# Kernel tuning notes

Measured on AMD Instinct MI355X. Metric: run time of the kernel, lower is better.

## Reference

```python
import jax, jax.numpy as jnp
import numpy as np

B, N, F, K = 16384, 64, 128, 64


def setup_inputs() -> dict:
    key = jax.random.key(0)
    kx, kd = jax.random.split(key)
    x = jax.random.normal(kx, (B, F), dtype=jnp.float32)
    D = jax.random.normal(kd, (N, F, K), dtype=jnp.float32)  # per-cluster factor dictionaries
    return {"x": x, "D": D}


def reference(x, D):
    # --- assignment step (torch.no_grad in original) ---
    # Dtx[n,b,j] = sum_i D[n,i,j] * x[b,i]
    Dtx = jnp.einsum('nij,bi->nbj', D, x)                      # [N,B,K]
    # per-cluster (D^T D)^{-1}, batched inverse over the cluster axis
    DTD = jnp.einsum('nij,nik->njk', D, D)                     # [N,K,K]
    DTD_inv = jnp.linalg.inv(DTD)                              # [N,K,K]
    Cs = jnp.einsum('nbj,nkj->nbk', Dtx, DTD_inv)              # [N,B,K]
    x_hat = jnp.einsum('nij,nbj->nbi', D, Cs)                  # [N,B,F]
    # nearest-subspace assignment per sample
    label = jnp.argmin(jnp.linalg.norm(x_hat - x[None], axis=-1), axis=0)  # [B] int
    C = Cs[label, jnp.arange(x.shape[0])]                      # [B,K] gather per sample
    # --- reconstruction loss: sum_i || x[i] - D[label[i]] @ C[i] ||^2 ---
    x_rec = jnp.einsum('bik,bk->bi', D[label], C)              # grouped gather + matmul
    se_loss = jnp.sum(jnp.square(x - x_rec))
    return se_loss, label
```

## Files before the change

### kernel.cpp

```cpp
#include <hip/hip_runtime.h>
#include <hip/hip_bf16.h>

#define B_N 16384
#define TAU 0.25f
#define GS 68
#define YS 132

typedef float f32x4 __attribute__((ext_vector_type(4)));
typedef short s16x8 __attribute__((ext_vector_type(8)));

__device__ __forceinline__ void gl_lds16(const void* g, void* l) {
    __builtin_amdgcn_global_load_lds(
        (const __attribute__((address_space(1))) void*)g,
        (__attribute__((address_space(3))) void*)l, 16, 0, 0);
}

__device__ __forceinline__ unsigned short bf16_bits(float v) {
    __hip_bfloat16 h = __float2bfloat16(v);
    return *reinterpret_cast<unsigned short*>(&h);
}

__global__ __launch_bounds__(256) void prep_convert(const float* __restrict__ x,
                                                    const float* __restrict__ D,
                                                    unsigned short* __restrict__ xh,
                                                    float* __restrict__ nrm,
                                                    float* __restrict__ Qg,
                                                    unsigned short* __restrict__ Bht,
                                                    float* __restrict__ out) {
    __shared__ __align__(16) float Y[64 * YS];
    __shared__ __align__(16) float G[64 * GS + 64];
    __shared__ __align__(16) float Lti[8 * 8 * 8];
    const int t = threadIdx.x;

    if (blockIdx.x >= 64) {
        const int gid = (blockIdx.x - 64) * 256 + t;
        if (gid == 0) out[0] = 0.0f;
        const size_t base = (size_t)gid * 64;
        float s = 0.0f;
        #pragma unroll
        for (int c = 0; c < 16; ++c) {
            const f32x4 v = ((const f32x4*)(x + base))[c];
            s += v.x * v.x + v.y * v.y + v.z * v.z + v.w * v.w;
            ushort4 h;
            h.x = bf16_bits(v.x); h.y = bf16_bits(v.y);
            h.z = bf16_bits(v.z); h.w = bf16_bits(v.w);
            ((ushort4*)(xh + base))[c] = h;
        }
        s += __shfl_xor(s, 1, 64);
        if ((gid & 1) == 0) nrm[gid >> 1] = s;
        return;
    }

    const int n = blockIdx.x;
    const float* Dn = D + (size_t)n * 8192;

    for (int e4 = t; e4 < 2048; e4 += 256) {
        const int c = e4 >> 4, j4 = (e4 & 15) * 4;
        const f32x4 v = ((const f32x4*)Dn)[e4];
        Y[(j4 + 0) * YS + c] = v.x;
        Y[(j4 + 1) * YS + c] = v.y;
        Y[(j4 + 2) * YS + c] = v.z;
        Y[(j4 + 3) * YS + c] = v.w;
    }
    __syncthreads();

    {
        const int a0 = (t & 15) * 4, b0 = (t >> 4) * 4;
        float acc[4][4] = {};
        for (int c4 = 0; c4 < 32; ++c4) {
            f32x4 A[4], Bv[4];
            #pragma unroll
            for (int p = 0; p < 4; ++p) {
                A[p]  = *(const f32x4*)&Y[(a0 + p) * YS + c4 * 4];
                Bv[p] = *(const f32x4*)&Y[(b0 + p) * YS + c4 * 4];
            }
            #pragma unroll
            for (int p = 0; p < 4; ++p)
                #pragma unroll
                for (int q = 0; q < 4; ++q)
                    acc[p][q] += A[p].x * Bv[q].x + A[p].y * Bv[q].y +
                                 A[p].z * Bv[q].z + A[p].w * Bv[q].w;
        }
        #pragma unroll
        for (int p = 0; p < 4; ++p)
            #pragma unroll
            for (int q = 0; q < 4; ++q) G[(a0 + p) * GS + b0 + q] = acc[p][q];
    }
    __syncthreads();

    for (int p8 = 0; p8 < 8; ++p8) {
        const int pb = p8 * 8;
        if (t < 64) {
            const int lane = t;
            const f32x4 v0 = *(const f32x4*)&G[lane * GS + pb];
            const f32x4 v1 = *(const f32x4*)&G[lane * GS + pb + 4];
            float g[8] = {v0.x, v0.y, v0.z, v0.w, v1.x, v1.y, v1.z, v1.w};
            #pragma unroll
            for (int kk = 0; kk < 8; ++kk) {
                const int k = pb + kk;
                const float dk = __shfl(g[kk], k, 64);
                const float rinv = 1.0f / sqrtf(dk);
                const float lik = g[kk] * rinv;
                g[kk] = lik;
                if (lane == 0) G[64 * GS + k] = rinv;
                #pragma unroll
                for (int jj = kk + 1; jj < 8; ++jj) {
                    const float ljk = __shfl(lik, pb + jj, 64);
                    g[jj] -= lik * ljk;
                }
            }
            *(f32x4*)&G[lane * GS + pb]     = (f32x4){g[0], g[1], g[2], g[3]};
            *(f32x4*)&G[lane * GS + pb + 4] = (f32x4){g[4], g[5], g[6], g[7]};
        }
        __syncthreads();
        const int base = pb + 8;
        if (base < 64) {
            for (int i = base + (t >> 5); i < 64; i += 8) {
                const f32x4 Li0 = *(const f32x4*)&G[i * GS + pb];
                const f32x4 Li1 = *(const f32x4*)&G[i * GS + pb + 4];
                for (int j = base + (t & 31); j < 64; j += 32) {
                    const f32x4 Lj0 = *(const f32x4*)&G[j * GS + pb];
                    const f32x4 Lj1 = *(const f32x4*)&G[j * GS + pb + 4];
                    float s = G[i * GS + j];
                    s -= Li0.x * Lj0.x + Li0.y * Lj0.y + Li0.z * Lj0.z + Li0.w * Lj0.w;
                    s -= Li1.x * Lj1.x + Li1.y * Lj1.y + Li1.z * Lj1.z + Li1.w * Lj1.w;
                    G[i * GS + j] = s;
                }
            }
        }
        __syncthreads();
    }

    if (t < 64) {
        const int bi = t >> 3, c = t & 7;
        const int base = bi * 8;
        float m[8];
        #pragma unroll
        for (int r = 0; r < 8; ++r) {
            float s = (r == c) ? 1.0f : 0.0f;
            #pragma unroll
            for (int k = 0; k < r; ++k)
                s -= G[(base + r) * GS + base + k] * m[k];
            m[r] = s * G[64 * GS + base + r];
        }
        #pragma unroll
        for (int r = 0; r < 8; ++r) Lti[(base + r) * 8 + c] = m[r];
    }
    __syncthreads();

    if (t < 128) {
        const int c = t;
        for (int i = 0; i < 8; ++i) {
            float Tv[8];
            #pragma unroll
            for (int r = 0; r < 8; ++r) Tv[r] = Y[(i * 8 + r) * YS + c];
            for (int k = 0; k < i; ++k) {
                #pragma unroll
                for (int kk = 0; kk < 8; ++kk) {
                    const float z = Y[(k * 8 + kk) * YS + c];
                    #pragma unroll
                    for (int r = 0; r < 8; ++r)
                        Tv[r] -= G[(i * 8 + r) * GS + k * 8 + kk] * z;
                }
            }
            #pragma unroll
            for (int r = 0; r < 8; ++r) {
                float z = 0.0f;
                #pragma unroll
                for (int rp = 0; rp <= r; ++rp)
                    z += Lti[(i * 8 + r) * 8 + rp] * Tv[rp];
                Y[(i * 8 + r) * YS + c] = z;
            }
        }
    }
    __syncthreads();

    for (int e = t; e < 8192; e += 256) {
        const int j = e >> 7, i = e & 127;
        Bht[((size_t)n * 64 + j) * 128 + i] = bf16_bits(Y[j * YS + i]);
    }
    for (int e = t; e < 8192; e += 256) {
        const int i = e >> 6, j = e & 63;
        Qg[(size_t)n * 8192 + e] = Y[j * YS + i];
    }
}

__global__ __launch_bounds__(256) void gemm_scores(const unsigned short* __restrict__ xh,
                                                   const unsigned short* __restrict__ Bht,
                                                   float* __restrict__ S) {
    __shared__ unsigned short ldsA[128 * 128];
    __shared__ unsigned short ldsB[128 * 128];
    const int t = threadIdx.x, w = t >> 6, lane = t & 63;
    const int m0 = blockIdx.x * 128;
    const int nsplit = blockIdx.y;
    const int wm = w & 1, wn = w >> 1;

    {
        const int rl = lane >> 4;
        const int p  = lane & 15;
        #pragma unroll
        for (int q = 0; q < 8; ++q) {
            const int row = w * 32 + q * 4 + rl;
            const int c = p ^ (row & 15);
            gl_lds16(xh + (size_t)(m0 + row) * 128 + c * 8,
                     &ldsA[(w * 32 + q * 4) * 128]);
            gl_lds16(Bht + (size_t)(nsplit * 1024 + row) * 128 + c * 8,
                     &ldsB[(w * 32 + q * 4) * 128]);
        }
    }
    __syncthreads();

    s16x8 af[4][4];
    #pragma unroll
    for (int mt = 0; mt < 4; ++mt) {
        const int r = wm * 64 + mt * 16 + (lane & 15);
        #pragma unroll
        for (int ks = 0; ks < 4; ++ks) {
            const int p = (ks * 4 + (lane >> 4)) ^ (lane & 15);
            af[mt][ks] = *(const s16x8*)&ldsA[r * 128 + p * 8];
        }
    }

    #pragma unroll 1
    for (int it = 0; it < 8; ++it) {
        s16x8 bf[4][4];
        #pragma unroll
        for (int nt = 0; nt < 4; ++nt) {
            const int r = wn * 64 + nt * 16 + (lane & 15);
            #pragma unroll
            for (int ks = 0; ks < 4; ++ks) {
                const int p = (ks * 4 + (lane >> 4)) ^ (lane & 15);
                bf[nt][ks] = *(const s16x8*)&ldsB[r * 128 + p * 8];
            }
        }
        __syncthreads();

        if (it < 7) {
            const int rl = lane >> 4, p = lane & 15;
            #pragma unroll
            for (int q = 0; q < 8; ++q) {
                const int row = w * 32 + q * 4 + rl;
                const int c = p ^ (row & 15);
                gl_lds16(Bht + (size_t)(nsplit * 1024 + (it + 1) * 128 + row) * 128 + c * 8,
                         &ldsB[(w * 32 + q * 4) * 128]);
            }
        }

        f32x4 acc[4][4];
        #pragma unroll
        for (int mt = 0; mt < 4; ++mt)
            #pragma unroll
            for (int nt = 0; nt < 4; ++nt) acc[mt][nt] = (f32x4){0.f, 0.f, 0.f, 0.f};
        #pragma unroll
        for (int ks = 0; ks < 4; ++ks)
            #pragma unroll
            for (int mt = 0; mt < 4; ++mt)
                #pragma unroll
                for (int nt = 0; nt < 4; ++nt)
                    acc[mt][nt] = __builtin_amdgcn_mfma_f32_16x16x32_bf16(
                        af[mt][ks], bf[nt][ks], acc[mt][nt], 0, 0, 0);

        const int nc = nsplit * 16 + it * 2 + wn;
        #pragma unroll
        for (int mt = 0; mt < 4; ++mt) {
            #pragma unroll
            for (int rg = 0; rg < 4; ++rg) {
                float p = 0.0f;
                #pragma unroll
                for (int nt = 0; nt < 4; ++nt) {
                    const float v = acc[mt][nt][rg];
                    p += v * v;
                }
                p += __shfl_xor(p, 1, 64);
                p += __shfl_xor(p, 2, 64);
                p += __shfl_xor(p, 4, 64);
                p += __shfl_xor(p, 8, 64);
                if ((lane & 15) == 0) {
                    const int m = wm * 64 + mt * 16 + (lane >> 4) * 4 + rg;
                    S[(size_t)nc * B_N + m0 + m] = p;
                }
            }
        }
        __syncthreads();
    }
}

__global__ __launch_bounds__(256) void argmax_rescore(const float* __restrict__ Sa,
                                                      const float* __restrict__ nrm,
                                                      const float* __restrict__ x,
                                                      const float* __restrict__ Qg,
                                                      float* __restrict__ out) {
    __shared__ float tile[64 * 65];
    __shared__ int sflags[64];
    __shared__ int scnt;
    __shared__ float ssum;
    __shared__ float scorr[4];
    const int t = threadIdx.x, w = t >> 6, lane = t & 63;
    const int b0 = blockIdx.x * 64;
    if (t == 0) scnt = 0;

    for (int idx = t; idx < 1024; idx += 256) {
        const int n = idx >> 4, c4 = idx & 15;
        const f32x4 v = *(const f32x4*)&Sa[(size_t)n * B_N + b0 + c4 * 4];
        tile[(c4 * 4 + 0) * 65 + n] = v.x;
        tile[(c4 * 4 + 1) * 65 + n] = v.y;
        tile[(c4 * 4 + 2) * 65 + n] = v.z;
        tile[(c4 * 4 + 3) * 65 + n] = v.w;
    }
    __syncthreads();

    if (t < 64) {
        float v1 = -1e30f, v2 = -1e30f;
        int n1 = 0;
        for (int n = 0; n < 64; ++n) {
            const float v = tile[t * 65 + n];
            if (v > v1) { v2 = v1; v1 = v; n1 = n; }
            else v2 = fmaxf(v2, v);
        }
        out[1 + b0 + t] = (float)n1;
        if (v1 - v2 < TAU) { const int i = atomicAdd(&scnt, 1); sflags[i] = t; }
        float err = nrm[b0 + t] - v1;
        for (int off = 32; off; off >>= 1) err += __shfl_xor(err, off, 64);
        if (t == 0) ssum = err;
    }
    if (lane == 0) scorr[w] = 0.0f;
    __syncthreads();

    const int nf = scnt;
    float corr = 0.0f;
    for (int f = w; f < nf; f += 4) {
        const int s = sflags[f];
        const int b2 = b0 + s;
        const float v = tile[s * 65 + lane];
        float vm = v;
        for (int off = 32; off; off >>= 1) vm = fmaxf(vm, __shfl_xor(vm, off, 64));
        unsigned long long mask = __ballot((vm - v) < TAU);
        float best = -1e30f;
        int bn = 0;
        while (mask) {
            const int nn = (int)__builtin_ctzll(mask);
            mask &= mask - 1;
            const float* Qn = Qg + (size_t)nn * 8192;
            const float* xb = x + (size_t)b2 * 128;
            float dot = 0.0f;
            #pragma unroll 8
            for (int i = 0; i < 128; ++i)
                dot = fmaf(Qn[i * 64 + lane], xb[i], dot);
            float sv = dot * dot;
            for (int off = 32; off; off >>= 1) sv += __shfl_xor(sv, off, 64);
            if (sv > best) { best = sv; bn = nn; }
        }
        if (lane == 0) {
            out[1 + b2] = (float)bn;
            corr += vm - best;
        }
    }
    if (lane == 0 && corr != 0.0f) scorr[w] += corr;
    __syncthreads();
    if (t == 0)
        atomicAdd(out, ssum + scorr[0] + scorr[1] + scorr[2] + scorr[3]);
}

extern "C" void kernel_launch(void* const* d_in, const int* in_sizes, int n_in,
                              void* d_out, int out_size, void* d_ws, size_t ws_size,
                              hipStream_t stream) {
    const float* x = (const float*)d_in[0];
    const float* D = (const float*)d_in[1];
    float* out = (float*)d_out;

    char* ws = (char*)d_ws;
    unsigned short* xh  = (unsigned short*)(ws);
    unsigned short* Bht = (unsigned short*)(ws + (4u << 20));
    float* Qg           = (float*)(ws + (5u << 20));
    float* Sa           = (float*)(ws + (7u << 20));
    float* nrm          = (float*)(ws + (11u << 20));

    prep_convert<<<192, 256, 0, stream>>>(x, D, xh, nrm, Qg, Bht, out);
    gemm_scores<<<dim3(128, 4), 256, 0, stream>>>(xh, Bht, Sa);
    argmax_rescore<<<256, 256, 0, stream>>>(Sa, nrm, x, Qg, out);
}
```

Before: 164.1 us.

## Split prep kernel, compute Gram from global, shrink MFMA accumulator live range

The combined prep/convert kernel is split into two launches: a convert kernel in which each thread handles 32 floats, and a per-cluster prep kernel. The D^T D Gram product now reads D directly from global memory with scalar FMAs, so the LDS transpose no longer feeds it and the barrier after the transpose is dropped. The Y pad changes to 133. In gemm_scores, MFMA accumulation moves inside the per-mt loop so only 4 accumulators stay live, which is meant to lower register pressure. The trade-offs are an extra kernel launch, and later readers of Y may lose the synchronisation they relied on.

```diff
diff --git a/kernel.cpp b/kernel.cpp
--- a/kernel.cpp
+++ b/kernel.cpp
@@ -4,7 +4,7 @@
 #define B_N 16384
 #define TAU 0.25f
 #define GS 68
-#define YS 132
+#define YS 133
 
 typedef float f32x4 __attribute__((ext_vector_type(4)));
 typedef short s16x8 __attribute__((ext_vector_type(8)));
@@ -20,37 +20,35 @@
     return *reinterpret_cast<unsigned short*>(&h);
 }
 
-__global__ __launch_bounds__(256) void prep_convert(const float* __restrict__ x,
-                                                    const float* __restrict__ D,
-                                                    unsigned short* __restrict__ xh,
-                                                    float* __restrict__ nrm,
-                                                    float* __restrict__ Qg,
-                                                    unsigned short* __restrict__ Bht,
-                                                    float* __restrict__ out) {
-    __shared__ __align__(16) float Y[64 * YS];
+__global__ __launch_bounds__(256) void convert_kernel(const float* __restrict__ x,
+                                                      unsigned short* __restrict__ xh,
+                                                      float* __restrict__ nrm,
+                                                      float* __restrict__ out) {
+    const int gid = blockIdx.x * 256 + threadIdx.x;
+    if (gid == 0) out[0] = 0.0f;
+    const size_t base = (size_t)gid * 32;
+    float s = 0.0f;
+    #pragma unroll
+    for (int c = 0; c < 8; ++c) {
+        const f32x4 v = ((const f32x4*)(x + base))[c];
+        s += v.x * v.x + v.y * v.y + v.z * v.z + v.w * v.w;
+        ushort4 h;
+        h.x = bf16_bits(v.x); h.y = bf16_bits(v.y);
+        h.z = bf16_bits(v.z); h.w = bf16_bits(v.w);
+        ((ushort4*)(xh + base))[c] = h;
+    }
+    s += __shfl_xor(s, 1, 64);
+    s += __shfl_xor(s, 2, 64);
+    if ((gid & 3) == 0) nrm[gid >> 2] = s;
+}
+
+__global__ __launch_bounds__(256) void prep_kernel(const float* __restrict__ D,
+                                                   float* __restrict__ Qg,
+                                                   unsigned short* __restrict__ Bht) {
+    __shared__ float Y[64 * YS];
     __shared__ __align__(16) float G[64 * GS + 64];
     __shared__ __align__(16) float Lti[8 * 8 * 8];
     const int t = threadIdx.x;
-
-    if (blockIdx.x >= 64) {
-        const int gid = (blockIdx.x - 64) * 256 + t;
-        if (gid == 0) out[0] = 0.0f;
-        const size_t base = (size_t)gid * 64;
-        float s = 0.0f;
-        #pragma unroll
-        for (int c = 0; c < 16; ++c) {
-            const f32x4 v = ((const f32x4*)(x + base))[c];
-            s += v.x * v.x + v.y * v.y + v.z * v.z + v.w * v.w;
-            ushort4 h;
-            h.x = bf16_bits(v.x); h.y = bf16_bits(v.y);
-            h.z = bf16_bits(v.z); h.w = bf16_bits(v.w);
-            ((ushort4*)(xh + base))[c] = h;
-        }
-        s += __shfl_xor(s, 1, 64);
-        if ((gid & 1) == 0) nrm[gid >> 1] = s;
-        return;
-    }
-
     const int n = blockIdx.x;
     const float* Dn = D + (size_t)n * 8192;
 
@@ -62,24 +60,20 @@
         Y[(j4 + 2) * YS + c] = v.z;
         Y[(j4 + 3) * YS + c] = v.w;
     }
-    __syncthreads();
 
     {
         const int a0 = (t & 15) * 4, b0 = (t >> 4) * 4;
         float acc[4][4] = {};
-        for (int c4 = 0; c4 < 32; ++c4) {
-            f32x4 A[4], Bv[4];
-            #pragma unroll
-            for (int p = 0; p < 4; ++p) {
-                A[p]  = *(const f32x4*)&Y[(a0 + p) * YS + c4 * 4];
-                Bv[p] = *(const f32x4*)&Y[(b0 + p) * YS + c4 * 4];
-            }
+        #pragma unroll 4
+        for (int i = 0; i < 128; ++i) {
+            const f32x4 av = *(const f32x4*)(Dn + i * 64 + a0);
+            const f32x4 bv = *(const f32x4*)(Dn + i * 64 + b0);
+            const float aa[4] = {av.x, av.y, av.z, av.w};
+            const float bb[4] = {bv.x, bv.y, bv.z, bv.w};
             #pragma unroll
             for (int p = 0; p < 4; ++p)
                 #pragma unroll
-                for (int q = 0; q < 4; ++q)
-                    acc[p][q] += A[p].x * Bv[q].x + A[p].y * Bv[q].y +
-                                 A[p].z * Bv[q].z + A[p].w * Bv[q].w;
+                for (int q = 0; q < 4; ++q) acc[p][q] = fmaf(aa[p], bb[q], acc[p][q]);
         }
         #pragma unroll
         for (int p = 0; p < 4; ++p)
@@ -246,29 +240,24 @@
             }
         }
 
-        f32x4 acc[4][4];
-        #pragma unroll
-        for (int mt = 0; mt < 4; ++mt)
-            #pragma unroll
-            for (int nt = 0; nt < 4; ++nt) acc[mt][nt] = (f32x4){0.f, 0.f, 0.f, 0.f};
-        #pragma unroll
-        for (int ks = 0; ks < 4; ++ks)
-            #pragma unroll
-            for (int mt = 0; mt < 4; ++mt)
+        const int nc = nsplit * 16 + it * 2 + wn;
+        #pragma unroll
+        for (int mt = 0; mt < 4; ++mt) {
+            f32x4 acc[4];
+            #pragma unroll
+            for (int nt = 0; nt < 4; ++nt) acc[nt] = (f32x4){0.f, 0.f, 0.f, 0.f};
+            #pragma unroll
+            for (int ks = 0; ks < 4; ++ks)
                 #pragma unroll
                 for (int nt = 0; nt < 4; ++nt)
-                    acc[mt][nt] = __builtin_amdgcn_mfma_f32_16x16x32_bf16(
-                        af[mt][ks], bf[nt][ks], acc[mt][nt], 0, 0, 0);
-
-        const int nc = nsplit * 16 + it * 2 + wn;
-        #pragma unroll
-        for (int mt = 0; mt < 4; ++mt) {
+                    acc[nt] = __builtin_amdgcn_mfma_f32_16x16x32_bf16(
+                        af[mt][ks], bf[nt][ks], acc[nt], 0, 0, 0);
             #pragma unroll
             for (int rg = 0; rg < 4; ++rg) {
                 float p = 0.0f;
                 #pragma unroll
                 for (int nt = 0; nt < 4; ++nt) {
-                    const float v = acc[mt][nt][rg];
+                    const float v = acc[nt][rg];
                     p += v * v;
                 }
                 p += __shfl_xor(p, 1, 64);
@@ -375,7 +364,8 @@
     float* Sa           = (float*)(ws + (7u << 20));
     float* nrm          = (float*)(ws + (11u << 20));
 
-    prep_convert<<<192, 256, 0, stream>>>(x, D, xh, nrm, Qg, Bht, out);
+    convert_kernel<<<256, 256, 0, stream>>>(x, xh, nrm, out);
+    prep_kernel<<<64, 256, 0, stream>>>(D, Qg, Bht);
     gemm_scores<<<dim3(128, 4), 256, 0, stream>>>(xh, Bht, Sa);
     argmax_rescore<<<256, 256, 0, stream>>>(Sa, nrm, x, Qg, out);
 }
```

New measurement: 168.2 us. 2.5% more time.
